# Kernel tuning notes

Measured on AMD Instinct MI355X. Metric: run time of the kernel, lower is better.

Reference implementation:

```python
import jax, jax.numpy as jnp
import numpy as np

N_NODES = 100000
HIDDEN = 128
N_EDGES = 1000000


def setup_inputs() -> dict:
    key = jax.random.key(0)
    k1, k2, k3, k4 = jax.random.split(key, 4)
    z = jax.random.normal(k1, (N_NODES, HIDDEN), dtype=jnp.float32)
    edge_label_index = jax.random.randint(k2, (2, N_EDGES), 0, N_NODES, dtype=jnp.int64)
    # Kaiming-ish scaled init for the two Linear layers (lin1: 2H->H, lin2: H->1)
    W1 = jax.random.normal(k3, (2 * HIDDEN, HIDDEN), dtype=jnp.float32) / np.sqrt(2 * HIDDEN)
    b1 = jnp.zeros((HIDDEN,), dtype=jnp.float32)
    W2 = jax.random.normal(k4, (HIDDEN, 1), dtype=jnp.float32) / np.sqrt(HIDDEN)
    b2 = jnp.zeros((1,), dtype=jnp.float32)
    return {"z": z, "edge_label_index": edge_label_index, "W1": W1, "b1": b1, "W2": W2, "b2": b2}


def reference(z, edge_label_index, W1, b1, W2, b2):
    row, col = edge_label_index[0], edge_label_index[1]
    # gather endpoint embeddings and concat: [E, 2H]
    h = jnp.concatenate([z[row], z[col]], axis=-1)
    h = jax.nn.relu(h @ W1 + b1)          # [E, H]
    out = h @ W2 + b2                     # [E, 1]
    return out.reshape(-1)
```

## Files before the change

kernel.cpp:

```cpp
#include <hip/hip_runtime.h>
#include <hip/hip_bf16.h>
#include <stdint.h>

#define HIDDEN 128
#define LDS_STRIDE 136

typedef __attribute__((ext_vector_type(8))) short short8;
typedef __attribute__((ext_vector_type(4))) unsigned uint4v;
typedef __attribute__((ext_vector_type(4))) float float4v;
typedef __attribute__((ext_vector_type(2))) float float2v;
typedef __attribute__((ext_vector_type(2))) unsigned uint2v;

static __device__ __forceinline__ unsigned short f2bf(float f) {
    union { float f; unsigned u; } v; v.f = f;
    unsigned r = (v.u + 0x7FFFu + ((v.u >> 16) & 1u)) >> 16;
    return (unsigned short)r;
}

static __device__ __forceinline__ unsigned pack2bf(float f0, float f1) {
    unsigned u0 = __float_as_uint(f0) + 0x8000u;
    unsigned u1 = __float_as_uint(f1) + 0x8000u;
    return __builtin_amdgcn_perm(u1, u0, 0x07060302u);
}

static __device__ __forceinline__ short8 pack8(float4v lo, float4v hi) {
    uint4v u;
    u[0] = pack2bf(lo[0], lo[1]);
    u[1] = pack2bf(lo[2], lo[3]);
    u[2] = pack2bf(hi[0], hi[1]);
    u[3] = pack2bf(hi[2], hi[3]);
    return *(short8*)&u;
}

__global__ void prep_wt(const float* __restrict__ W1, const float* __restrict__ b1,
                        const float* __restrict__ W2,
                        unsigned short* __restrict__ Wt,
                        float* __restrict__ b1p, float* __restrict__ W2p) {
    int idx = blockIdx.x * blockDim.x + threadIdx.x;
    if (idx < 256 * 128) {
        int j = idx >> 7, k = idx & 127;
        float v = (j < 128) ? W1[k * 128 + j] : W1[(128 + k) * 128 + (j - 128)];
        Wt[idx] = f2bf(v);
    }
    if (idx < 128) {
        int m = idx >> 3, tt = idx & 7;
        int jj = tt * 16 + m;
        b1p[idx] = b1[jj];
        W2p[idx] = W2[jj];
    }
}

__global__ __launch_bounds__(512) void node_gemm(
        const float* __restrict__ z, const unsigned short* __restrict__ Wt,
        const float* __restrict__ b1p,
        unsigned short* __restrict__ Q, int n_nodes) {
    __shared__ unsigned short Wl[128 * LDS_STRIDE];

    int tid  = threadIdx.x;
    int h    = blockIdx.x & 1;

    #pragma unroll
    for (int i = 0; i < 4; ++i) {
        int chunk = tid + i * 512;
        int c  = chunk >> 4;
        int k0 = (chunk & 15) * 8;
        short8 v = *(const short8*)(Wt + h * 16384 + chunk * 8);
        *(short8*)(Wl + c * LDS_STRIDE + k0) = v;
    }
    __syncthreads();

    int lane = tid & 63;
    int wave = tid >> 6;
    int m    = lane & 15;
    int quad = lane >> 4;

    float4v b1a = (float4v)(0.0f), b1b = (float4v)(0.0f);
    if (h == 0) {
        b1a = *(const float4v*)(b1p + m * 8);
        b1b = *(const float4v*)(b1p + m * 8 + 4);
    }

    int nTiles = (n_nodes + 15) >> 4;
    int tileStride = (gridDim.x >> 1) * 8;

    for (int tile = (blockIdx.x >> 1) * 8 + wave; tile < nTiles; tile += tileStride) {
        int nodebase = tile * 16;
        int row = nodebase + m;

        short8 a[4];
        {
            bool ok = row < n_nodes;
            const float* zp = z + (size_t)row * HIDDEN + quad * 8;
            #pragma unroll
            for (int s = 0; s < 4; ++s) {
                float4v z0 = ok ? *(const float4v*)(zp + s * 32)     : (float4v)(0.0f);
                float4v z1 = ok ? *(const float4v*)(zp + s * 32 + 4) : (float4v)(0.0f);
                a[s] = pack8(z0, z1);
            }
        }

        float4v acc[8];
        #pragma unroll
        for (int t = 0; t < 8; ++t) acc[t] = (float4v)(0.0f);

        #pragma unroll
        for (int t = 0; t < 8; ++t) {
            const unsigned short* wp = Wl + (t * 16 + m) * LDS_STRIDE + quad * 8;
            #pragma unroll
            for (int s = 0; s < 4; ++s) {
                short8 b = *(const short8*)(wp + s * 32);
                acc[t] = __builtin_amdgcn_mfma_f32_16x16x32_bf16(a[s], b, acc[t], 0, 0, 0);
            }
        }

        #pragma unroll
        for (int r = 0; r < 4; ++r) {
            int node = nodebase + quad * 4 + r;
            if (node < n_nodes) {
                uint4v pk;
                pk[0] = pack2bf(acc[0][r] + b1a[0], acc[1][r] + b1a[1]);
                pk[1] = pack2bf(acc[2][r] + b1a[2], acc[3][r] + b1a[3]);
                pk[2] = pack2bf(acc[4][r] + b1b[0], acc[5][r] + b1b[1]);
                pk[3] = pack2bf(acc[6][r] + b1b[2], acc[7][r] + b1b[3]);
                *(uint4v*)(Q + (size_t)node * 256 + h * 128 + m * 8) = pk;
            }
        }
    }
}

__global__ __launch_bounds__(256) void edge_kernel(
        const int* __restrict__ eli, const unsigned short* __restrict__ Q,
        const float* __restrict__ W2p, const float* __restrict__ b2,
        float* __restrict__ out, int E) {
    int g      = threadIdx.x >> 4;
    int lane16 = threadIdx.x & 15;
    int j0 = lane16 * 8;

    float2v w[4];
    #pragma unroll
    for (int k = 0; k < 4; ++k) w[k] = ((const float2v*)(W2p + j0))[k];
    float bias2 = b2[0];

    int e0 = blockIdx.x * 64 + g;

    int idx_r[4], idx_c[4];
    #pragma unroll
    for (int i = 0; i < 4; ++i) {
        int e = e0 + i * 16;
        idx_r[i] = (e < E) ? eli[e]     : 0;
        idx_c[i] = (e < E) ? eli[E + e] : 0;
    }

    uint4v u1[4], u2[4];
    #pragma unroll
    for (int i = 0; i < 4; ++i) {
        u1[i] = *(const uint4v*)(Q + (size_t)idx_r[i] * 256 + j0);
        u2[i] = *(const uint4v*)(Q + (size_t)idx_c[i] * 256 + 128 + j0);
    }

    #pragma unroll
    for (int i = 0; i < 4; ++i) {
        float2v accv = (float2v)(0.0f);
        #pragma unroll
        for (int k = 0; k < 4; ++k) {
            unsigned a1 = u1[i][k], a2 = u2[i][k];
            float2v v1, v2;
            v1[0] = __uint_as_float(a1 << 16);
            v1[1] = __uint_as_float(a1 & 0xFFFF0000u);
            v2[0] = __uint_as_float(a2 << 16);
            v2[1] = __uint_as_float(a2 & 0xFFFF0000u);
            float2v s = v1 + v2;
            s[0] = fmaxf(s[0], 0.0f);
            s[1] = fmaxf(s[1], 0.0f);
            accv[0] = fmaf(s[0], w[k][0], accv[0]);
            accv[1] = fmaf(s[1], w[k][1], accv[1]);
        }
        float acc = accv[0] + accv[1];
        acc += __shfl_xor(acc, 1);
        acc += __shfl_xor(acc, 2);
        acc += __shfl_xor(acc, 4);
        acc += __shfl_xor(acc, 8);

        int e = e0 + i * 16;
        if (lane16 == 0 && e < E) out[e] = acc + bias2;
    }
}

extern "C" void kernel_launch(void* const* d_in, const int* in_sizes, int n_in,
                              void* d_out, int out_size, void* d_ws, size_t ws_size,
                              hipStream_t stream) {
    const float* z   = (const float*)d_in[0];
    const int*   eli = (const int*)d_in[1];
    const float* W1  = (const float*)d_in[2];
    const float* b1  = (const float*)d_in[3];
    const float* W2  = (const float*)d_in[4];
    const float* b2  = (const float*)d_in[5];
    int n_nodes = in_sizes[0] / HIDDEN;
    int E       = in_sizes[1] / 2;
    float* out  = (float*)d_out;

    size_t qbytes = (size_t)n_nodes * 256 * 2;
    unsigned short* Q   = (unsigned short*)d_ws;
    unsigned short* Wt  = (unsigned short*)((char*)d_ws + qbytes);
    float*          b1p = (float*)((char*)d_ws + qbytes + 256 * 128 * 2);
    float*          W2p = b1p + 128;

    prep_wt<<<128, 256, 0, stream>>>(W1, b1, W2, Wt, b1p, W2p);

    node_gemm<<<1024, 512, 0, stream>>>(z, Wt, b1p, Q, n_nodes);

    edge_kernel<<<(E + 63) / 64, 256, 0, stream>>>(eli, Q, W2p, b2, out, E);
}
```

Baseline: 183.9 us.

## Bucket-sort edges by source node before gathering endpoint projections

Adds a counting sort of edges into 16-node buckets keyed on the row index (histogram, single-block scan, atomic scatter), then runs a sorted edge kernel that writes results back through a permutation. The aim is better locality for the row-side gathers of Q. In exchange it adds four extra launches plus a memset, atomics, and roughly 12 MB of extra index traffic. The output writes become scattered, and the single-block scan runs serially.

Result: slower. 290.3 us (+57.9%).

```diff
diff --git a/kernel.cpp b/kernel.cpp
--- a/kernel.cpp
+++ b/kernel.cpp
@@ -47,6 +47,45 @@
         int jj = tt * 16 + m;
         b1p[idx] = b1[jj];
         W2p[idx] = W2[jj];
+    }
+}
+
+__global__ void edge_hist(const int* __restrict__ eli, int E, int* __restrict__ cnt) {
+    int i = blockIdx.x * 256 + threadIdx.x;
+    if (i < E) atomicAdd(&cnt[eli[i] >> 4], 1);
+}
+
+__global__ void bucket_scan(int* __restrict__ cnt, int* __restrict__ off, int nb) {
+    __shared__ int part[256];
+    int t = threadIdx.x;
+    int per = (nb + 255) / 256;
+    int s = 0;
+    for (int i = 0; i < per; ++i) {
+        int idx = t * per + i;
+        if (idx < nb) s += cnt[idx];
+    }
+    part[t] = s;
+    __syncthreads();
+    if (t == 0) {
+        int acc = 0;
+        for (int i = 0; i < 256; ++i) { int v = part[i]; part[i] = acc; acc += v; }
+    }
+    __syncthreads();
+    int base = part[t];
+    for (int i = 0; i < per; ++i) {
+        int idx = t * per + i;
+        if (idx < nb) { int v = cnt[idx]; off[idx] = base; base += v; }
+    }
+}
+
+__global__ void edge_scatter(const int* __restrict__ eli, int E, int* __restrict__ cur,
+                             int* __restrict__ sr, int* __restrict__ sc,
+                             int* __restrict__ se) {
+    int i = blockIdx.x * 256 + threadIdx.x;
+    if (i < E) {
+        int r = eli[i], c = eli[E + i];
+        int p = atomicAdd(&cur[r >> 4], 1);
+        sr[p] = r; sc[p] = c; se[p] = i;
     }
 }
 
@@ -128,6 +167,70 @@
     }
 }
 
+static __device__ __forceinline__ float edge_dot(uint4v u1, uint4v u2, const float2v* w) {
+    float2v accv = (float2v)(0.0f);
+    #pragma unroll
+    for (int k = 0; k < 4; ++k) {
+        unsigned a1 = u1[k], a2 = u2[k];
+        float2v v1, v2;
+        v1[0] = __uint_as_float(a1 << 16);
+        v1[1] = __uint_as_float(a1 & 0xFFFF0000u);
+        v2[0] = __uint_as_float(a2 << 16);
+        v2[1] = __uint_as_float(a2 & 0xFFFF0000u);
+        float2v s = v1 + v2;
+        s[0] = fmaxf(s[0], 0.0f);
+        s[1] = fmaxf(s[1], 0.0f);
+        accv[0] = fmaf(s[0], w[k][0], accv[0]);
+        accv[1] = fmaf(s[1], w[k][1], accv[1]);
+    }
+    return accv[0] + accv[1];
+}
+
+__global__ __launch_bounds__(256) void edge_kernel_sorted(
+        const int* __restrict__ sr, const int* __restrict__ sc,
+        const int* __restrict__ se, const unsigned short* __restrict__ Q,
+        const float* __restrict__ W2p, const float* __restrict__ b2,
+        float* __restrict__ out, int E) {
+    int g      = threadIdx.x >> 4;
+    int lane16 = threadIdx.x & 15;
+    int j0 = lane16 * 8;
+
+    float2v w[4];
+    #pragma unroll
+    for (int k = 0; k < 4; ++k) w[k] = ((const float2v*)(W2p + j0))[k];
+    float bias2 = b2[0];
+
+    int e0 = blockIdx.x * 64 + g;
+
+    int idx_r[4], idx_c[4], oe[4];
+    #pragma unroll
+    for (int i = 0; i < 4; ++i) {
+        int e = e0 + i * 16;
+        bool ok = e < E;
+        idx_r[i] = ok ? sr[e] : 0;
+        idx_c[i] = ok ? sc[e] : 0;
+        oe[i]    = ok ? se[e] : 0;
+    }
+
+    uint4v u1[4], u2[4];
+    #pragma unroll
+    for (int i = 0; i < 4; ++i) {
+        u1[i] = *(const uint4v*)(Q + (size_t)idx_r[i] * 256 + j0);
+        u2[i] = *(const uint4v*)(Q + (size_t)idx_c[i] * 256 + 128 + j0);
+    }
+
+    #pragma unroll
+    for (int i = 0; i < 4; ++i) {
+        float acc = edge_dot(u1[i], u2[i], w);
+        acc += __shfl_xor(acc, 1);
+        acc += __shfl_xor(acc, 2);
+        acc += __shfl_xor(acc, 4);
+        acc += __shfl_xor(acc, 8);
+        int e = e0 + i * 16;
+        if (lane16 == 0 && e < E) out[oe[i]] = acc + bias2;
+    }
+}
+
 __global__ __launch_bounds__(256) void edge_kernel(
         const int* __restrict__ eli, const unsigned short* __restrict__ Q,
         const float* __restrict__ W2p, const float* __restrict__ b2,
@@ -160,27 +263,11 @@
 
     #pragma unroll
     for (int i = 0; i < 4; ++i) {
-        float2v accv = (float2v)(0.0f);
-        #pragma unroll
-        for (int k = 0; k < 4; ++k) {
-            unsigned a1 = u1[i][k], a2 = u2[i][k];
-            float2v v1, v2;
-            v1[0] = __uint_as_float(a1 << 16);
-            v1[1] = __uint_as_float(a1 & 0xFFFF0000u);
-            v2[0] = __uint_as_float(a2 << 16);
-            v2[1] = __uint_as_float(a2 & 0xFFFF0000u);
-            float2v s = v1 + v2;
-            s[0] = fmaxf(s[0], 0.0f);
-            s[1] = fmaxf(s[1], 0.0f);
-            accv[0] = fmaf(s[0], w[k][0], accv[0]);
-            accv[1] = fmaf(s[1], w[k][1], accv[1]);
-        }
-        float acc = accv[0] + accv[1];
+        float acc = edge_dot(u1[i], u2[i], w);
         acc += __shfl_xor(acc, 1);
         acc += __shfl_xor(acc, 2);
         acc += __shfl_xor(acc, 4);
         acc += __shfl_xor(acc, 8);
-
         int e = e0 + i * 16;
         if (lane16 == 0 && e < E) out[e] = acc + bias2;
     }
@@ -199,15 +286,35 @@
     int E       = in_sizes[1] / 2;
     float* out  = (float*)d_out;
 
-    size_t qbytes = (size_t)n_nodes * 256 * 2;
-    unsigned short* Q   = (unsigned short*)d_ws;
-    unsigned short* Wt  = (unsigned short*)((char*)d_ws + qbytes);
-    float*          b1p = (float*)((char*)d_ws + qbytes + 256 * 128 * 2);
-    float*          W2p = b1p + 128;
+    int nb = (n_nodes + 15) >> 4;
+
+    size_t off = 0;
+    unsigned short* Q   = (unsigned short*)d_ws;           off += (size_t)n_nodes * 256 * 2;
+    unsigned short* Wt  = (unsigned short*)((char*)d_ws + off); off += 256 * 128 * 2;
+    float*          b1p = (float*)((char*)d_ws + off);     off += 128 * 4;
+    float*          W2p = (float*)((char*)d_ws + off);     off += 128 * 4;
+    off = (off + 255) & ~(size_t)255;
+    int* sr  = (int*)((char*)d_ws + off);                  off += (size_t)E * 4;
+    int* sc  = (int*)((char*)d_ws + off);                  off += (size_t)E * 4;
+    int* se  = (int*)((char*)d_ws + off);                  off += (size_t)E * 4;
+    int* cnt = (int*)((char*)d_ws + off);                  off += (size_t)nb * 4;
+    int* cur = (int*)((char*)d_ws + off);                  off += (size_t)nb * 4;
+    bool use_sort = (off <= ws_size);
 
     prep_wt<<<128, 256, 0, stream>>>(W1, b1, W2, Wt, b1p, W2p);
 
+    if (use_sort) {
+        hipMemsetAsync(cnt, 0, (size_t)nb * 4, stream);
+        edge_hist<<<(E + 255) / 256, 256, 0, stream>>>(eli, E, cnt);
+        bucket_scan<<<1, 256, 0, stream>>>(cnt, cur, nb);
+        edge_scatter<<<(E + 255) / 256, 256, 0, stream>>>(eli, E, cur, sr, sc, se);
+    }
+
     node_gemm<<<1024, 512, 0, stream>>>(z, Wt, b1p, Q, n_nodes);
 
-    edge_kernel<<<(E + 63) / 64, 256, 0, stream>>>(eli, Q, W2p, b2, out, E);
-}
+    if (use_sort) {
+        edge_kernel_sorted<<<(E + 63) / 64, 256, 0, stream>>>(sr, sc, se, Q, W2p, b2, out, E);
+    } else {
+        edge_kernel<<<(E + 63) / 64, 256, 0, stream>>>(eli, Q, W2p, b2, out, E);
+    }
+}
```

## Quantize per-node projected features to int8 with per-row scales

Applied to the files above, without the earlier changes.

The node GEMM now writes its projected hidden features as 8-bit unsigned codes with a per-node, per-half absmax scale, where it used to write bf16. The edge kernel gathers these smaller rows plus two scalar scales and dequantizes inline before the ReLU and the W2 dot product. This halves the bytes of random gather traffic per edge, which is the dominant cost. It also lowers accuracy to roughly 8-bit precision on the pre-activation values and adds scale gathers.

Measured after the change: 163.0 us. -11.4%, faster.

```diff
diff --git a/kernel.cpp b/kernel.cpp
--- a/kernel.cpp
+++ b/kernel.cpp
@@ -53,7 +53,8 @@
 __global__ __launch_bounds__(512) void node_gemm(
         const float* __restrict__ z, const unsigned short* __restrict__ Wt,
         const float* __restrict__ b1p,
-        unsigned short* __restrict__ Q, int n_nodes) {
+        unsigned char* __restrict__ Qi, float* __restrict__ sA, float* __restrict__ sB,
+        int n_nodes) {
     __shared__ unsigned short Wl[128 * LDS_STRIDE];
 
     int tid  = threadIdx.x;
@@ -79,6 +80,7 @@
         b1a = *(const float4v*)(b1p + m * 8);
         b1b = *(const float4v*)(b1p + m * 8 + 4);
     }
+    float* sArr = (h == 0) ? sA : sB;
 
     int nTiles = (n_nodes + 15) >> 4;
     int tileStride = (gridDim.x >> 1) * 8;
@@ -116,29 +118,56 @@
         #pragma unroll
         for (int r = 0; r < 4; ++r) {
             int node = nodebase + quad * 4 + r;
+            float v[8];
+            v[0] = acc[0][r] + b1a[0]; v[1] = acc[1][r] + b1a[1];
+            v[2] = acc[2][r] + b1a[2]; v[3] = acc[3][r] + b1a[3];
+            v[4] = acc[4][r] + b1b[0]; v[5] = acc[5][r] + b1b[1];
+            v[6] = acc[6][r] + b1b[2]; v[7] = acc[7][r] + b1b[3];
+
+            float amax = fabsf(v[0]);
+            #pragma unroll
+            for (int t = 1; t < 8; ++t) amax = fmaxf(amax, fabsf(v[t]));
+            amax = fmaxf(amax, __shfl_xor(amax, 1));
+            amax = fmaxf(amax, __shfl_xor(amax, 2));
+            amax = fmaxf(amax, __shfl_xor(amax, 4));
+            amax = fmaxf(amax, __shfl_xor(amax, 8));
+            amax = fmaxf(amax, 1e-30f);
+
+            float inv = 126.5f * __builtin_amdgcn_rcpf(amax);
+            float s   = amax * (1.0f / 126.5f);
+
+            unsigned d0 = 0, d1 = 0;
+            #pragma unroll
+            for (int t = 0; t < 4; ++t) {
+                int q = (int)rintf(fmaf(v[t], inv, 128.0f));
+                d0 |= ((unsigned)q & 255u) << (8 * t);
+            }
+            #pragma unroll
+            for (int t = 0; t < 4; ++t) {
+                int q = (int)rintf(fmaf(v[4 + t], inv, 128.0f));
+                d1 |= ((unsigned)q & 255u) << (8 * t);
+            }
+
             if (node < n_nodes) {
-                uint4v pk;
-                pk[0] = pack2bf(acc[0][r] + b1a[0], acc[1][r] + b1a[1]);
-                pk[1] = pack2bf(acc[2][r] + b1a[2], acc[3][r] + b1a[3]);
-                pk[2] = pack2bf(acc[4][r] + b1b[0], acc[5][r] + b1b[1]);
-                pk[3] = pack2bf(acc[6][r] + b1b[2], acc[7][r] + b1b[3]);
-                *(uint4v*)(Q + (size_t)node * 256 + h * 128 + m * 8) = pk;
+                uint2v pk; pk[0] = d0; pk[1] = d1;
+                *(uint2v*)(Qi + (size_t)node * 256 + h * 128 + m * 8) = pk;
+                if (m == 0) sArr[node] = s;
             }
         }
     }
 }
 
 __global__ __launch_bounds__(256) void edge_kernel(
-        const int* __restrict__ eli, const unsigned short* __restrict__ Q,
+        const int* __restrict__ eli, const unsigned char* __restrict__ Qi,
+        const float* __restrict__ sA, const float* __restrict__ sB,
         const float* __restrict__ W2p, const float* __restrict__ b2,
         float* __restrict__ out, int E) {
     int g      = threadIdx.x >> 4;
     int lane16 = threadIdx.x & 15;
     int j0 = lane16 * 8;
 
-    float2v w[4];
-    #pragma unroll
-    for (int k = 0; k < 4; ++k) w[k] = ((const float2v*)(W2p + j0))[k];
+    float4v wA = *(const float4v*)(W2p + j0);
+    float4v wB = *(const float4v*)(W2p + j0 + 4);
     float bias2 = b2[0];
 
     int e0 = blockIdx.x * 64 + g;
@@ -151,31 +180,40 @@
         idx_c[i] = (e < E) ? eli[E + e] : 0;
     }
 
-    uint4v u1[4], u2[4];
-    #pragma unroll
-    for (int i = 0; i < 4; ++i) {
-        u1[i] = *(const uint4v*)(Q + (size_t)idx_r[i] * 256 + j0);
-        u2[i] = *(const uint4v*)(Q + (size_t)idx_c[i] * 256 + 128 + j0);
-    }
-
-    #pragma unroll
-    for (int i = 0; i < 4; ++i) {
-        float2v accv = (float2v)(0.0f);
+    uint2v u1[4], u2[4];
+    float s1[4], s2[4];
+    #pragma unroll
+    for (int i = 0; i < 4; ++i) {
+        u1[i] = *(const uint2v*)(Qi + (size_t)idx_r[i] * 256 + j0);
+        u2[i] = *(const uint2v*)(Qi + (size_t)idx_c[i] * 256 + 128 + j0);
+        s1[i] = sA[idx_r[i]];
+        s2[i] = sB[idx_c[i]];
+    }
+
+    #pragma unroll
+    for (int i = 0; i < 4; ++i) {
+        float a1 = s1[i], a2 = s2[i];
+        float off = -128.0f * (a1 + a2);
+        float acc = 0.0f;
+        unsigned da = u1[i][0], db = u2[i][0];
         #pragma unroll
         for (int k = 0; k < 4; ++k) {
-            unsigned a1 = u1[i][k], a2 = u2[i][k];
-            float2v v1, v2;
-            v1[0] = __uint_as_float(a1 << 16);
-            v1[1] = __uint_as_float(a1 & 0xFFFF0000u);
-            v2[0] = __uint_as_float(a2 << 16);
-            v2[1] = __uint_as_float(a2 & 0xFFFF0000u);
-            float2v s = v1 + v2;
-            s[0] = fmaxf(s[0], 0.0f);
-            s[1] = fmaxf(s[1], 0.0f);
-            accv[0] = fmaf(s[0], w[k][0], accv[0]);
-            accv[1] = fmaf(s[1], w[k][1], accv[1]);
-        }
-        float acc = accv[0] + accv[1];
+            float af = (float)((da >> (8 * k)) & 255u);
+            float bf = (float)((db >> (8 * k)) & 255u);
+            float v = fmaf(a2, bf, fmaf(a1, af, off));
+            v = fmaxf(v, 0.0f);
+            acc = fmaf(v, wA[k], acc);
+        }
+        da = u1[i][1]; db = u2[i][1];
+        #pragma unroll
+        for (int k = 0; k < 4; ++k) {
+            float af = (float)((da >> (8 * k)) & 255u);
+            float bf = (float)((db >> (8 * k)) & 255u);
+            float v = fmaf(a2, bf, fmaf(a1, af, off));
+            v = fmaxf(v, 0.0f);
+            acc = fmaf(v, wB[k], acc);
+        }
+
         acc += __shfl_xor(acc, 1);
         acc += __shfl_xor(acc, 2);
         acc += __shfl_xor(acc, 4);
@@ -199,15 +237,17 @@
     int E       = in_sizes[1] / 2;
     float* out  = (float*)d_out;
 
-    size_t qbytes = (size_t)n_nodes * 256 * 2;
-    unsigned short* Q   = (unsigned short*)d_ws;
-    unsigned short* Wt  = (unsigned short*)((char*)d_ws + qbytes);
-    float*          b1p = (float*)((char*)d_ws + qbytes + 256 * 128 * 2);
-    float*          W2p = b1p + 128;
+    size_t off = 0;
+    unsigned char* Qi  = (unsigned char*)d_ws;              off += (size_t)n_nodes * 256;
+    unsigned short* Wt = (unsigned short*)((char*)d_ws + off); off += 256 * 128 * 2;
+    float* b1p = (float*)((char*)d_ws + off);               off += 128 * 4;
+    float* W2p = (float*)((char*)d_ws + off);               off += 128 * 4;
+    float* sA  = (float*)((char*)d_ws + off);               off += (size_t)n_nodes * 4;
+    float* sB  = (float*)((char*)d_ws + off);               off += (size_t)n_nodes * 4;
 
     prep_wt<<<128, 256, 0, stream>>>(W1, b1, W2, Wt, b1p, W2p);
 
-    node_gemm<<<1024, 512, 0, stream>>>(z, Wt, b1p, Q, n_nodes);
-
-    edge_kernel<<<(E + 63) / 64, 256, 0, stream>>>(eli, Q, W2p, b2, out, E);
-}
+    node_gemm<<<1024, 512, 0, stream>>>(z, Wt, b1p, Qi, sA, sB, n_nodes);
+
+    edge_kernel<<<(E + 63) / 64, 256, 0, stream>>>(eli, Qi, sA, sB, W2p, b2, out, E);
+}
```
